# Kernel tuning notes

Hardware: AMD Instinct MI355X
Metric: run time of the kernel (lower is better)

## Reference

```python
import jax, jax.numpy as jnp
import numpy as np

B, S, DIM, SDIM = 4, 4096, 1024, 256


def setup_inputs() -> dict:
    key = jax.random.key(0)
    ks = jax.random.split(key, 10)
    def lin(k, din, dout):
        return jax.random.normal(k, (din, dout), jnp.float32) / np.float32(np.sqrt(din))
    return {
        "x": jax.random.normal(ks[0], (B, S, DIM), jnp.float32),
        "ln_g": jnp.ones((DIM,), jnp.float32),
        "ln_b": jnp.zeros((DIM,), jnp.float32),
        "mix_w": jax.random.normal(ks[1], (DIM, 1, 3), jnp.float32) * 0.3,  # depthwise conv kernel
        "mix_b": jnp.zeros((DIM,), jnp.float32),
        "Wi": lin(ks[2], DIM, DIM), "bi": jnp.zeros((DIM,), jnp.float32),
        "Wsin": lin(ks[3], DIM, SDIM), "bsin": jnp.zeros((SDIM,), jnp.float32),
        "Wd": lin(ks[4], DIM, SDIM), "bd": jnp.zeros((SDIM,), jnp.float32),
        "Wsel": lin(ks[5], DIM, SDIM), "bsel": jnp.zeros((SDIM,), jnp.float32),
        "Wso": lin(ks[6], SDIM, DIM), "bso": jnp.zeros((DIM,), jnp.float32),
        "Wg": lin(ks[7], DIM, DIM), "bg": jnp.zeros((DIM,), jnp.float32),
        "Wout": lin(ks[8], DIM, DIM), "bout": jnp.zeros((DIM,), jnp.float32),
    }


def reference(x, ln_g, ln_b, mix_w, mix_b, Wi, bi, Wsin, bsin, Wd, bd,
              Wsel, bsel, Wso, bso, Wg, bg, Wout, bout):
    eps = 1e-5
    # LayerNorm over last dim
    mu = jnp.mean(x, axis=-1, keepdims=True)
    var = jnp.mean(jnp.square(x - mu), axis=-1, keepdims=True)
    h = (x - mu) * jax.lax.rsqrt(var + eps) * ln_g + ln_b
    # depthwise Conv1d, kernel=3, padding=1, groups=dim
    hc = jnp.transpose(h, (0, 2, 1))  # [B, C, L]
    mixed = jax.lax.conv_general_dilated(
        hc, mix_w, window_strides=(1,), padding=[(1, 1)],
        dimension_numbers=("NCH", "OIH", "NCH"), feature_group_count=hc.shape[1])
    mixed = jnp.transpose(mixed + mix_b[None, :, None], (0, 2, 1))  # [B, S, D]
    u = jnp.tanh(mixed @ Wi + bi)                 # [B, S, D]
    x_state = jnp.tanh(mixed @ Wsin + bsin)       # [B, S, N]
    decay = jax.nn.sigmoid(mixed @ Wd + bd)       # [B, S, N]
    select = jax.nn.sigmoid(mixed @ Wsel + bsel)  # [B, S, N]
    # sequential linear recurrence: state = d*state + (1-d)*x_state
    def step(state, inp):
        dt, xt = inp
        state = dt * state + (1.0 - dt) * xt
        return state, state
    init = jnp.zeros((x.shape[0], x_state.shape[-1]), x.dtype)
    _, states = jax.lax.scan(step, init,
                             (jnp.swapaxes(decay, 0, 1), jnp.swapaxes(x_state, 0, 1)))
    states = jnp.swapaxes(states, 0, 1)           # [B, S, N]
    y = (select * states) @ Wso + bso             # [B, S, D]
    g = jax.nn.sigmoid(mixed @ Wg + bg)
    out = (g * y + (1.0 - g) * u) @ Wout + bout
    return x + out
```

## Files before the change

### kernel.cpp

```cpp
#include <hip/hip_runtime.h>
#include <hip/hip_bf16.h>
#include <math.h>

typedef __bf16 bf16_t;
typedef __bf16 bf16x8 __attribute__((ext_vector_type(8)));
typedef __bf16 bf16x4 __attribute__((ext_vector_type(4)));
typedef float  f32x4  __attribute__((ext_vector_type(4)));

#define B_ 4
#define S_ 4096
#define D_ 1024
#define N_ 256
#define M_ (B_*S_)

__device__ __forceinline__ float fsig(float x){
    return __builtin_amdgcn_rcpf(1.0f + __expf(-x));
}
__device__ __forceinline__ float ftanh(float x){
    return 1.0f - 2.0f*__builtin_amdgcn_rcpf(1.0f + __expf(2.0f*x));
}

__device__ __forceinline__ void gload_lds16(const void* g, void* l){
    __builtin_amdgcn_global_load_lds(
        (const __attribute__((address_space(1))) unsigned int*)g,
        (__attribute__((address_space(3))) unsigned int*)l, 16, 0, 0);
}

struct TJobs {
    const float* in[7];
    bf16_t*      out[7];
    int R[7];
    int C[7];
};

__global__ void transpose_all(TJobs j){
    int z = blockIdx.z;
    int R = j.R[z], C = j.C[z];
    int c0 = blockIdx.x*32, r0 = blockIdx.y*32;
    if (c0 >= C || r0 >= R) return;
    __shared__ float tile[32][33];
    int tx = threadIdx.x, ty = threadIdx.y;
    const float* in = j.in[z];
    bf16_t* out = j.out[z];
    #pragma unroll
    for (int i=0;i<32;i+=8)
        tile[ty+i][tx] = in[(size_t)(r0+ty+i)*C + (c0+tx)];
    __syncthreads();
    #pragma unroll
    for (int i=0;i<32;i+=8)
        out[(size_t)(c0+ty+i)*R + (r0+tx)] = (bf16_t)tile[tx][ty+i];
}

__global__ void ln_kernel(const float* __restrict__ x, const float* __restrict__ gw,
                          const float* __restrict__ bw, bf16_t* __restrict__ h){
    int row = blockIdx.x;
    int t = threadIdx.x;
    float4 v = ((const float4*)(x + (size_t)row*D_))[t];
    float s = v.x+v.y+v.z+v.w;
    float q = v.x*v.x+v.y*v.y+v.z*v.z+v.w*v.w;
    #pragma unroll
    for (int o=1;o<64;o<<=1){ s += __shfl_xor(s,o,64); q += __shfl_xor(q,o,64); }
    __shared__ float sw[4], sq[4];
    int wid = t>>6;
    if ((t&63)==0){ sw[wid]=s; sq[wid]=q; }
    __syncthreads();
    s = sw[0]+sw[1]+sw[2]+sw[3];
    q = sq[0]+sq[1]+sq[2]+sq[3];
    float mu = s*(1.0f/D_);
    float rs = rsqrtf(q*(1.0f/D_) - mu*mu + 1e-5f);
    float4 gv = ((const float4*)gw)[t];
    float4 bv = ((const float4*)bw)[t];
    bf16x4 o4;
    o4[0] = (bf16_t)((v.x-mu)*rs*gv.x + bv.x);
    o4[1] = (bf16_t)((v.y-mu)*rs*gv.y + bv.y);
    o4[2] = (bf16_t)((v.z-mu)*rs*gv.z + bv.z);
    o4[3] = (bf16_t)((v.w-mu)*rs*gv.w + bv.w);
    *(bf16x4*)(h + (size_t)row*D_ + t*4) = o4;
}

__global__ void conv_kernel(const bf16_t* __restrict__ h, const float* __restrict__ w,
                            const float* __restrict__ mb, bf16_t* __restrict__ mix){
    int idx = blockIdx.x*256 + threadIdx.x;
    int g8  = idx & 127;
    int row = idx >> 7;
    int s   = row & (S_-1);
    int d0  = g8*8;
    const bf16_t* hr = h + (size_t)row*D_ + d0;
    bf16x8 cur = *(const bf16x8*)hr;
    bf16x8 prv, nxt;
    #pragma unroll
    for (int i=0;i<8;i++){ prv[i]=(bf16_t)0.0f; nxt[i]=(bf16_t)0.0f; }
    if (s > 0)      prv = *(const bf16x8*)(hr - D_);
    if (s < S_-1)   nxt = *(const bf16x8*)(hr + D_);
    bf16x8 ov;
    #pragma unroll
    for (int i=0;i<8;i++){
        int d = d0+i;
        float o = (float)prv[i]*w[d*3] + (float)cur[i]*w[d*3+1] + (float)nxt[i]*w[d*3+2] + mb[d];
        ov[i] = (bf16_t)o;
    }
    *(bf16x8*)(mix + (size_t)row*D_ + d0) = ov;
}

struct Epi {
    const float *b0,*b1,*b2,*b3,*b4;
    bf16_t *u, *g, *z;
    bf16_t *xs, *dc, *sel;
    const bf16_t *gbuf, *ubuf;
    const float *resid;
    float *outp;
};

#define WAITV3()  asm volatile("s_waitcnt vmcnt(3)" ::: "memory")
#define WAITV0()  asm volatile("s_waitcnt vmcnt(0)" ::: "memory")
#define WAITLGK0() asm volatile("s_waitcnt lgkmcnt(0)" ::: "memory")
#define CFENCE()  asm volatile("" ::: "memory")
#define BARR()    __builtin_amdgcn_s_barrier()

template<int MODE>
__global__ __launch_bounds__(512,4)
void gemm128(const bf16_t* __restrict__ A, const bf16_t* __restrict__ Bt,
             int K, Epi e){
    __shared__ __align__(16) char lds[73728];
    int t = threadIdx.x;
    int wave = t>>6, lane = t&63;
    int wm = (wave>>2)*64;
    int wn = (wave&3)*64;
    int lm = lane&15, quad = lane>>4;

    int m0 = blockIdx.x*128;
    int n0 = blockIdx.y*256;
    int NT = K>>5;

    const bf16_t* gA = A  + (size_t)(m0 + (t>>2))*K + (t&3)*8;
    const bf16_t* gB = Bt + (size_t)(n0 + (t>>2))*K + (t&3)*8;

    auto stage = [&](int kt){
        int x = kt % 3;
        const bf16_t* a = gA + kt*32;
        const bf16_t* b = gB + kt*32;
        char* da = lds + x*8192  + t*16;
        char* db = lds + 24576 + x*16384 + t*16;
        gload_lds16(a, da);
        gload_lds16(b, db);
        gload_lds16(b + (size_t)128*K, db + 8192);
    };

    int raBase = (wm+lm)*64 + quad*16;
    int rbBase = (wn+lm)*64 + quad*16;

    f32x4 acc[4][4];
    #pragma unroll
    for (int i=0;i<4;i++)
        #pragma unroll
        for (int j=0;j<4;j++)
            #pragma unroll
            for (int r=0;r<4;r++) acc[i][j][r]=0.0f;

    bf16x8 aF[4], bF[4];

    stage(0);
    stage(1);
    stage(2);
    WAITV3();
    BARR();
    CFENCE();
    {
        const char* pa = lds + raBase;
        const char* pb = lds + 24576 + rbBase;
        #pragma unroll
        for (int j=0;j<4;j++) bF[j] = *(const bf16x8*)(pb + j*1024);
        #pragma unroll
        for (int i=0;i<4;i++) aF[i] = *(const bf16x8*)(pa + i*1024);
    }

    for (int kt=0; kt<NT; ++kt){
        WAITLGK0();
        BARR();
        CFENCE();
        if (kt+3 < NT){
            stage(kt+3);
            WAITV3();
        } else {
            WAITV0();
        }
        CFENCE();

        bool more = (kt+1 < NT);
        int xn = (kt+1) % 3;
        const char* pan = lds + xn*8192  + raBase;
        const char* pbn = lds + 24576 + xn*16384 + rbBase;

        #pragma unroll
        for (int j=0;j<4;j++){
            #pragma unroll
            for (int i=0;i<4;i++)
                acc[i][j] = __builtin_amdgcn_mfma_f32_16x16x32_bf16(aF[i], bF[j], acc[i][j], 0,0,0);
            if (more) bF[j] = *(const bf16x8*)(pbn + j*1024);
        }
        if (more){
            #pragma unroll
            for (int i=0;i<4;i++) aF[i] = *(const bf16x8*)(pan + i*1024);
        }
    }
    __syncthreads();

    if (MODE==0 || MODE==1){
        const float* bp = e.b0; int cbase = 0; bf16_t* dst = 0; int width = D_;
        bool ut = true;
        if (MODE==0){
            ut = (n0 < 1280);
            if (n0 < 1024){ bp=e.b0; cbase=n0; dst=e.u; width=D_; }
            else if (n0 < 1792){
                int sub=(n0-1024)>>8;
                bp  = sub==0? e.b1 : sub==1? e.b2 : e.b3;
                dst = sub==0? e.xs : sub==1? e.dc : e.sel;
                cbase = 0; width = N_;
            } else { bp=e.b4; cbase=n0-1792; dst=e.g; width=D_; }
        } else {
            bp = e.b0; cbase = n0; width = D_;
        }
        bf16_t* Tb = (bf16_t*)lds;
        #pragma unroll
        for (int h=0; h<2; h++){
            if (h) __syncthreads();
            if (wm == h*64){
                #pragma unroll
                for (int ii=0;ii<4;ii++){
                    #pragma unroll
                    for (int j=0;j<4;j++){
                        float bv = bp[(MODE==0?cbase:n0) + wn + j*16 + lm];
                        #pragma unroll
                        for (int r=0;r<4;r++){
                            float v = acc[ii][j][r] + bv;
                            if (MODE==0) v = ut ? ftanh(v) : fsig(v);
                            Tb[(ii*16+quad*4+r)*260 + wn + j*16 + lm] = (bf16_t)v;
                        }
                    }
                }
            }
            __syncthreads();
            if (MODE==0){
                #pragma unroll
                for (int it=0; it<4; it++){
                    int idx = it*512 + t;
                    int row = idx>>5, c8 = idx&31;
                    bf16x8 v = *(const bf16x8*)&Tb[row*260 + c8*8];
                    *(bf16x8*)&dst[(size_t)(m0 + h*64 + row)*width + cbase + c8*8] = v;
                }
            } else {
                #pragma unroll
                for (int it=0; it<4; it++){
                    int idx = it*512 + t;
                    int row = idx>>5, c8 = idx&31;
                    bf16x8 y = *(const bf16x8*)&Tb[row*260 + c8*8];
                    size_t gi = (size_t)(m0 + h*64 + row)*D_ + n0 + c8*8;
                    bf16x8 gv = *(const bf16x8*)&e.gbuf[gi];
                    bf16x8 uv = *(const bf16x8*)&e.ubuf[gi];
                    bf16x8 o;
                    #pragma unroll
                    for (int q=0;q<8;q++){
                        float gf = (float)gv[q];
                        o[q] = (bf16_t)(gf*(float)y[q] + (1.0f-gf)*(float)uv[q]);
                    }
                    *(bf16x8*)&e.z[gi] = o;
                }
            }
        }
    } else {
        float* T = (float*)lds;
        #pragma unroll
        for (int pZ=0; pZ<4; pZ++){
            if (pZ) __syncthreads();
            if (wm == (pZ>>1)*64){
                int ib = (pZ&1)*2;
                #pragma unroll
                for (int ii=0;ii<2;ii++){
                    #pragma unroll
                    for (int j=0;j<4;j++)
                        #pragma unroll
                        for (int r=0;r<4;r++)
                            T[(ii*16+quad*4+r)*260 + wn + j*16 + lm] = acc[ib+ii][j][r];
                }
            }
            __syncthreads();
            #pragma unroll
            for (int it=0; it<4; it++){
                int idx = it*512 + t;
                int row = idx>>6, c4 = idx&63;
                f32x4 v = *(const f32x4*)&T[row*260 + c4*4];
                size_t gi = (size_t)(m0 + pZ*32 + row)*D_ + n0 + c4*4;
                float4 res = *(const float4*)&e.resid[gi];
                float4 bb  = *(const float4*)&e.b0[n0 + c4*4];
                float4 o;
                o.x = v[0]+res.x+bb.x; o.y = v[1]+res.y+bb.y;
                o.z = v[2]+res.z+bb.z; o.w = v[3]+res.w+bb.w;
                *(float4*)&e.outp[gi] = o;
            }
        }
    }
}

__global__ void scan_p1(const bf16_t* __restrict__ dc, const bf16_t* __restrict__ xs,
                        float* __restrict__ aggA, float* __restrict__ aggB){
    int wg4 = blockIdx.x*4 + (threadIdx.x>>6);
    int b = wg4>>6, ch = wg4&63;
    int l4 = (threadIdx.x&63)*4;
    size_t base = ((size_t)b*S_ + ch*64)*N_ + l4;
    float A0=1.f,A1=1.f,A2=1.f,A3=1.f, B0=0.f,B1=0.f,B2=0.f,B3=0.f;
    for (int t=0;t<64;t++){
        bf16x4 d4 = *(const bf16x4*)(dc + base + (size_t)t*N_);
        bf16x4 x4 = *(const bf16x4*)(xs + base + (size_t)t*N_);
        float d;
        d=(float)d4[0]; A0*=d; B0=d*B0+(1.f-d)*(float)x4[0];
        d=(float)d4[1]; A1*=d; B1=d*B1+(1.f-d)*(float)x4[1];
        d=(float)d4[2]; A2*=d; B2=d*B2+(1.f-d)*(float)x4[2];
        d=(float)d4[3]; A3*=d; B3=d*B3+(1.f-d)*(float)x4[3];
    }
    size_t o = (size_t)wg4*N_ + l4;
    float4 av; av.x=A0; av.y=A1; av.z=A2; av.w=A3;
    float4 bv; bv.x=B0; bv.y=B1; bv.z=B2; bv.w=B3;
    *(float4*)(aggA+o) = av;
    *(float4*)(aggB+o) = bv;
}

__global__ void scan_p2(const float* __restrict__ aggA, const float* __restrict__ aggB,
                        float* __restrict__ pre){
    int b = blockIdx.x, n = threadIdx.x;
    float s = 0.0f;
    for (int ch=0; ch<64; ch++){
        size_t i = ((size_t)b*64+ch)*N_+n;
        pre[i] = s;
        s = aggA[i]*s + aggB[i];
    }
}

__global__ void scan_p3(const bf16_t* __restrict__ dc, const bf16_t* __restrict__ xs,
                        const bf16_t* __restrict__ sel, const float* __restrict__ pre,
                        bf16_t* __restrict__ ss){
    int wg4 = blockIdx.x*4 + (threadIdx.x>>6);
    int b = wg4>>6, ch = wg4&63;
    int l4 = (threadIdx.x&63)*4;
    size_t base = ((size_t)b*S_ + ch*64)*N_ + l4;
    size_t o = (size_t)wg4*N_ + l4;
    float4 pv = *(const float4*)(pre+o);
    float s0=pv.x, s1=pv.y, s2=pv.z, s3=pv.w;
    for (int t=0;t<64;t++){
        size_t i = base + (size_t)t*N_;
        bf16x4 d4 = *(const bf16x4*)(dc+i);
        bf16x4 x4 = *(const bf16x4*)(xs+i);
        bf16x4 e4 = *(const bf16x4*)(sel+i);
        float d;
        d=(float)d4[0]; s0=d*s0+(1.f-d)*(float)x4[0];
        d=(float)d4[1]; s1=d*s1+(1.f-d)*(float)x4[1];
        d=(float)d4[2]; s2=d*s2+(1.f-d)*(float)x4[2];
        d=(float)d4[3]; s3=d*s3+(1.f-d)*(float)x4[3];
        bf16x4 o4;
        o4[0]=(bf16_t)((float)e4[0]*s0);
        o4[1]=(bf16_t)((float)e4[1]*s1);
        o4[2]=(bf16_t)((float)e4[2]*s2);
        o4[3]=(bf16_t)((float)e4[3]*s3);
        *(bf16x4*)(ss+i) = o4;
    }
}

extern "C" void kernel_launch(void* const* d_in, const int* in_sizes, int n_in,
                              void* d_out, int out_size, void* d_ws, size_t ws_size,
                              hipStream_t stream){
    const float* x    = (const float*)d_in[0];
    const float* ln_g = (const float*)d_in[1];
    const float* ln_b = (const float*)d_in[2];
    const float* mixw = (const float*)d_in[3];
    const float* mixb = (const float*)d_in[4];
    const float* Wi   = (const float*)d_in[5];
    const float* bi   = (const float*)d_in[6];
    const float* Wsin = (const float*)d_in[7];
    const float* bsin = (const float*)d_in[8];
    const float* Wd   = (const float*)d_in[9];
    const float* bd   = (const float*)d_in[10];
    const float* Wsel = (const float*)d_in[11];
    const float* bsel = (const float*)d_in[12];
    const float* Wso  = (const float*)d_in[13];
    const float* bso  = (const float*)d_in[14];
    const float* Wg   = (const float*)d_in[15];
    const float* bg   = (const float*)d_in[16];
    const float* Wout = (const float*)d_in[17];
    const float* bout = (const float*)d_in[18];
    float* out = (float*)d_out;

    char* p = (char*)d_ws;
    auto alloc = [&](size_t bytes)->char*{ char* r=p; p += (bytes+255)&~(size_t)255; return r; };
    bf16_t* hB    = (bf16_t*)alloc((size_t)M_*D_*2);
    bf16_t* mixB  = (bf16_t*)alloc((size_t)M_*D_*2);
    bf16_t* uB    = (bf16_t*)alloc((size_t)M_*D_*2);
    bf16_t* gB    = (bf16_t*)alloc((size_t)M_*D_*2);
    bf16_t* ssB   = (bf16_t*)alloc((size_t)M_*N_*2);
    bf16_t* xs    = (bf16_t*)alloc((size_t)M_*N_*2);
    bf16_t* dc    = (bf16_t*)alloc((size_t)M_*N_*2);
    bf16_t* sel   = (bf16_t*)alloc((size_t)M_*N_*2);
    bf16_t* WbigT = (bf16_t*)alloc((size_t)2816*1024*2);
    bf16_t* WsoT  = (bf16_t*)alloc(1024*256*2);
    bf16_t* WoutT = (bf16_t*)alloc(1024*1024*2);
    float*  aggA  = (float*)alloc((size_t)4*64*256*4);
    float*  aggB  = (float*)alloc((size_t)4*64*256*4);
    float*  pre   = (float*)alloc((size_t)4*64*256*4);
    bf16_t* zB = mixB;

    TJobs tj;
    tj.in[0]=Wi;   tj.out[0]=WbigT;            tj.R[0]=1024; tj.C[0]=1024;
    tj.in[1]=Wsin; tj.out[1]=WbigT+1024*1024;  tj.R[1]=1024; tj.C[1]=256;
    tj.in[2]=Wd;   tj.out[2]=WbigT+1280*1024;  tj.R[2]=1024; tj.C[2]=256;
    tj.in[3]=Wsel; tj.out[3]=WbigT+1536*1024;  tj.R[3]=1024; tj.C[3]=256;
    tj.in[4]=Wg;   tj.out[4]=WbigT+(size_t)1792*1024; tj.R[4]=1024; tj.C[4]=1024;
    tj.in[5]=Wso;  tj.out[5]=WsoT;             tj.R[5]=256;  tj.C[5]=1024;
    tj.in[6]=Wout; tj.out[6]=WoutT;            tj.R[6]=1024; tj.C[6]=1024;
    transpose_all<<<dim3(32,32,7), dim3(32,8), 0, stream>>>(tj);

    ln_kernel  <<<M_, 256, 0, stream>>>(x, ln_g, ln_b, hB);
    conv_kernel<<<M_*128/256, 256, 0, stream>>>(hB, mixw, mixb, mixB);

    Epi e0 = {};
    e0.b0=bi; e0.b1=bsin; e0.b2=bd; e0.b3=bsel; e0.b4=bg;
    e0.u=uB; e0.g=gB; e0.xs=xs; e0.dc=dc; e0.sel=sel;
    gemm128<0><<<dim3(M_/128, 11), 512, 0, stream>>>(mixB, WbigT, 1024, e0);

    scan_p1<<<64, 256, 0, stream>>>(dc, xs, aggA, aggB);
    scan_p2<<<4,  256, 0, stream>>>(aggA, aggB, pre);
    scan_p3<<<64, 256, 0, stream>>>(dc, xs, sel, pre, ssB);

    Epi e1 = {};
    e1.b0=bso; e1.gbuf=gB; e1.ubuf=uB; e1.z=zB;
    gemm128<1><<<dim3(M_/128, 4), 512, 0, stream>>>(ssB, WsoT, 256, e1);

    Epi e2 = {};
    e2.b0=bout; e2.resid=x; e2.outp=out;
    gemm128<2><<<dim3(M_/128, 4), 512, 0, stream>>>(zB, WoutT, 1024, e2);
}
```

Measured before the change: 402.3 us.

## Load GEMM B fragments directly from global in pre-swizzled layout; parallelize scan_p2

The weight transposes now write the bf16 weights in a k-grouped-by-8 layout, so each lane can read its MFMA B fragment straight from global memory (cached) instead of staging B through LDS. This shrinks LDS per block from 72KB to 34KB, which allows more resident blocks, and cuts the global-to-LDS traffic per k-step. The cost is that B reads now pay global/L2 latency inside the MFMA loop, and the vmcnt wait thresholds were adjusted to cover them. Separately, scan_p2 is rewritten as a wave-level parallel prefix scan over the 64 chunks using shuffles, one wave per (batch, state) chain, replacing the 64-step serial loop.

```diff
diff --git a/kernel.cpp b/kernel.cpp
--- a/kernel.cpp
+++ b/kernel.cpp
@@ -31,6 +31,8 @@
     bf16_t*      out[7];
     int R[7];
     int C[7];
+    int ldn[7];
+    int nf[7];
 };
 
 __global__ void transpose_all(TJobs j){
@@ -42,13 +44,16 @@
     int tx = threadIdx.x, ty = threadIdx.y;
     const float* in = j.in[z];
     bf16_t* out = j.out[z];
+    int ldn = j.ldn[z], nf = j.nf[z];
     #pragma unroll
     for (int i=0;i<32;i+=8)
         tile[ty+i][tx] = in[(size_t)(r0+ty+i)*C + (c0+tx)];
     __syncthreads();
     #pragma unroll
-    for (int i=0;i<32;i+=8)
-        out[(size_t)(c0+ty+i)*R + (r0+tx)] = (bf16_t)tile[tx][ty+i];
+    for (int i=0;i<32;i+=8){
+        int r = r0+tx, c = c0+ty+i;
+        out[((size_t)(r>>3)*ldn + nf + c)*8 + (r&7)] = (bf16_t)tile[tx][ty+i];
+    }
 }
 
 __global__ void ln_kernel(const float* __restrict__ x, const float* __restrict__ gw,
@@ -111,7 +116,7 @@
     float *outp;
 };
 
-#define WAITV3()  asm volatile("s_waitcnt vmcnt(3)" ::: "memory")
+#define WAITV5()  asm volatile("s_waitcnt vmcnt(5)" ::: "memory")
 #define WAITV0()  asm volatile("s_waitcnt vmcnt(0)" ::: "memory")
 #define WAITLGK0() asm volatile("s_waitcnt lgkmcnt(0)" ::: "memory")
 #define CFENCE()  asm volatile("" ::: "memory")
@@ -120,8 +125,8 @@
 template<int MODE>
 __global__ __launch_bounds__(512,4)
 void gemm128(const bf16_t* __restrict__ A, const bf16_t* __restrict__ Bt,
-             int K, Epi e){
-    __shared__ __align__(16) char lds[73728];
+             int K, int NB, Epi e){
+    __shared__ __align__(16) char lds[34816];
     int t = threadIdx.x;
     int wave = t>>6, lane = t&63;
     int wm = (wave>>2)*64;
@@ -132,22 +137,16 @@
     int n0 = blockIdx.y*256;
     int NT = K>>5;
 
-    const bf16_t* gA = A  + (size_t)(m0 + (t>>2))*K + (t&3)*8;
-    const bf16_t* gB = Bt + (size_t)(n0 + (t>>2))*K + (t&3)*8;
+    const bf16_t* gA = A + (size_t)(m0 + (t>>2))*K + (t&3)*8;
+    const bf16_t* gBq = Bt + ((size_t)quad*NB + n0 + wn + lm)*8;
+    const size_t ktStep = (size_t)32*NB;
 
     auto stage = [&](int kt){
-        int x = kt % 3;
-        const bf16_t* a = gA + kt*32;
-        const bf16_t* b = gB + kt*32;
-        char* da = lds + x*8192  + t*16;
-        char* db = lds + 24576 + x*16384 + t*16;
-        gload_lds16(a, da);
-        gload_lds16(b, db);
-        gload_lds16(b + (size_t)128*K, db + 8192);
+        char* da = lds + (kt%3)*8192 + t*16;
+        gload_lds16(gA + kt*32, da);
     };
 
     int raBase = (wm+lm)*64 + quad*16;
-    int rbBase = (wn+lm)*64 + quad*16;
 
     f32x4 acc[4][4];
     #pragma unroll
@@ -162,14 +161,13 @@
     stage(0);
     stage(1);
     stage(2);
-    WAITV3();
+    WAITV0();
     BARR();
     CFENCE();
+    #pragma unroll
+    for (int j=0;j<4;j++) bF[j] = *(const bf16x8*)(gBq + j*128);
     {
         const char* pa = lds + raBase;
-        const char* pb = lds + 24576 + rbBase;
-        #pragma unroll
-        for (int j=0;j<4;j++) bF[j] = *(const bf16x8*)(pb + j*1024);
         #pragma unroll
         for (int i=0;i<4;i++) aF[i] = *(const bf16x8*)(pa + i*1024);
     }
@@ -180,23 +178,22 @@
         CFENCE();
         if (kt+3 < NT){
             stage(kt+3);
-            WAITV3();
+            WAITV5();
         } else {
             WAITV0();
         }
         CFENCE();
 
         bool more = (kt+1 < NT);
-        int xn = (kt+1) % 3;
-        const char* pan = lds + xn*8192  + raBase;
-        const char* pbn = lds + 24576 + xn*16384 + rbBase;
+        const char* pan = lds + ((kt+1)%3)*8192 + raBase;
+        const bf16_t* gBn = gBq + (size_t)(kt+1)*ktStep;
 
         #pragma unroll
         for (int j=0;j<4;j++){
             #pragma unroll
             for (int i=0;i<4;i++)
                 acc[i][j] = __builtin_amdgcn_mfma_f32_16x16x32_bf16(aF[i], bF[j], acc[i][j], 0,0,0);
-            if (more) bF[j] = *(const bf16x8*)(pbn + j*1024);
+            if (more) bF[j] = *(const bf16x8*)(gBn + j*128);
         }
         if (more){
             #pragma unroll
@@ -326,13 +323,20 @@
 
 __global__ void scan_p2(const float* __restrict__ aggA, const float* __restrict__ aggB,
                         float* __restrict__ pre){
-    int b = blockIdx.x, n = threadIdx.x;
-    float s = 0.0f;
-    for (int ch=0; ch<64; ch++){
-        size_t i = ((size_t)b*64+ch)*N_+n;
-        pre[i] = s;
-        s = aggA[i]*s + aggB[i];
-    }
+    int chain = blockIdx.x*4 + (threadIdx.x>>6);
+    int lane  = threadIdx.x & 63;
+    int b = chain>>8, n = chain&255;
+    size_t i = ((size_t)b*64 + lane)*N_ + n;
+    float A = aggA[i], Bv = aggB[i];
+    #pragma unroll
+    for (int off=1; off<64; off<<=1){
+        float Ap = __shfl_up(A, off, 64);
+        float Bp = __shfl_up(Bv, off, 64);
+        if (lane >= off){ Bv = A*Bp + Bv; A = A*Ap; }
+    }
+    float preB = __shfl_up(Bv, 1, 64);
+    if (lane == 0) preB = 0.0f;
+    pre[i] = preB;
 }
 
 __global__ void scan_p3(const bf16_t* __restrict__ dc, const bf16_t* __restrict__ xs,
@@ -407,13 +411,13 @@
     bf16_t* zB = mixB;
 
     TJobs tj;
-    tj.in[0]=Wi;   tj.out[0]=WbigT;            tj.R[0]=1024; tj.C[0]=1024;
-    tj.in[1]=Wsin; tj.out[1]=WbigT+1024*1024;  tj.R[1]=1024; tj.C[1]=256;
-    tj.in[2]=Wd;   tj.out[2]=WbigT+1280*1024;  tj.R[2]=1024; tj.C[2]=256;
-    tj.in[3]=Wsel; tj.out[3]=WbigT+1536*1024;  tj.R[3]=1024; tj.C[3]=256;
-    tj.in[4]=Wg;   tj.out[4]=WbigT+(size_t)1792*1024; tj.R[4]=1024; tj.C[4]=1024;
-    tj.in[5]=Wso;  tj.out[5]=WsoT;             tj.R[5]=256;  tj.C[5]=1024;
-    tj.in[6]=Wout; tj.out[6]=WoutT;            tj.R[6]=1024; tj.C[6]=1024;
+    tj.in[0]=Wi;   tj.out[0]=WbigT; tj.R[0]=1024; tj.C[0]=1024; tj.ldn[0]=2816; tj.nf[0]=0;
+    tj.in[1]=Wsin; tj.out[1]=WbigT; tj.R[1]=1024; tj.C[1]=256;  tj.ldn[1]=2816; tj.nf[1]=1024;
+    tj.in[2]=Wd;   tj.out[2]=WbigT; tj.R[2]=1024; tj.C[2]=256;  tj.ldn[2]=2816; tj.nf[2]=1280;
+    tj.in[3]=Wsel; tj.out[3]=WbigT; tj.R[3]=1024; tj.C[3]=256;  tj.ldn[3]=2816; tj.nf[3]=1536;
+    tj.in[4]=Wg;   tj.out[4]=WbigT; tj.R[4]=1024; tj.C[4]=1024; tj.ldn[4]=2816; tj.nf[4]=1792;
+    tj.in[5]=Wso;  tj.out[5]=WsoT;  tj.R[5]=256;  tj.C[5]=1024; tj.ldn[5]=1024; tj.nf[5]=0;
+    tj.in[6]=Wout; tj.out[6]=WoutT; tj.R[6]=1024; tj.C[6]=1024; tj.ldn[6]=1024; tj.nf[6]=0;
     transpose_all<<<dim3(32,32,7), dim3(32,8), 0, stream>>>(tj);
 
     ln_kernel  <<<M_, 256, 0, stream>>>(x, ln_g, ln_b, hB);
@@ -422,17 +426,17 @@
     Epi e0 = {};
     e0.b0=bi; e0.b1=bsin; e0.b2=bd; e0.b3=bsel; e0.b4=bg;
     e0.u=uB; e0.g=gB; e0.xs=xs; e0.dc=dc; e0.sel=sel;
-    gemm128<0><<<dim3(M_/128, 11), 512, 0, stream>>>(mixB, WbigT, 1024, e0);
-
-    scan_p1<<<64, 256, 0, stream>>>(dc, xs, aggA, aggB);
-    scan_p2<<<4,  256, 0, stream>>>(aggA, aggB, pre);
-    scan_p3<<<64, 256, 0, stream>>>(dc, xs, sel, pre, ssB);
+    gemm128<0><<<dim3(M_/128, 11), 512, 0, stream>>>(mixB, WbigT, 1024, 2816, e0);
+
+    scan_p1<<<64,  256, 0, stream>>>(dc, xs, aggA, aggB);
+    scan_p2<<<256, 256, 0, stream>>>(aggA, aggB, pre);
+    scan_p3<<<64,  256, 0, stream>>>(dc, xs, sel, pre, ssB);
 
     Epi e1 = {};
     e1.b0=bso; e1.gbuf=gB; e1.ubuf=uB; e1.z=zB;
-    gemm128<1><<<dim3(M_/128, 4), 512, 0, stream>>>(ssB, WsoT, 256, e1);
+    gemm128<1><<<dim3(M_/128, 4), 512, 0, stream>>>(ssB, WsoT, 256, 1024, e1);
 
     Epi e2 = {};
     e2.b0=bout; e2.resid=x; e2.outp=out;
-    gemm128<2><<<dim3(M_/128, 4), 512, 0, stream>>>(zB, WoutT, 1024, e2);
-}
+    gemm128<2><<<dim3(M_/128, 4), 512, 0, stream>>>(zB, WoutT, 1024, 1024, e2);
+}
```

After: 384.7 us. 4.4% less time.
